# Performance work log

Hardware: AMD Instinct MI355X
Metric: run time of the kernel (lower is better)

Reference implementation:

```python
import jax, jax.numpy as jnp
import numpy as np

N_EMBD = 1024
N_HEAD = 16
HEAD_DIM = N_EMBD // N_HEAD


def setup_inputs() -> dict:
    key = jax.random.key(0)
    ks = jax.random.split(key, 5)
    B, S = 2, 2048
    scale = 0.02
    return {
        "hidden_states": jax.random.normal(ks[0], (B, S, N_EMBD), dtype=jnp.float32),
        "w_attn": jax.random.normal(ks[1], (N_EMBD, 3 * N_EMBD), dtype=jnp.float32) * scale,
        "b_attn": jnp.zeros((3 * N_EMBD,), dtype=jnp.float32),
        "w_proj": jax.random.normal(ks[2], (N_EMBD, N_EMBD), dtype=jnp.float32) * scale,
        "b_proj": jnp.zeros((N_EMBD,), dtype=jnp.float32),
    }


def reference(hidden_states, w_attn, b_attn, w_proj, b_proj):
    B, S, _ = hidden_states.shape
    qkv = hidden_states @ w_attn + b_attn                     # [B,S,3E]
    q, k, v = jnp.split(qkv, 3, axis=-1)                      # each [B,S,E]

    def split_heads(t):  # [B,S,E] -> [B,H,S,D]
        return t.reshape(B, S, N_HEAD, HEAD_DIM).transpose(0, 2, 1, 3)

    q, k, v = split_heads(q), split_heads(k), split_heads(v)

    scores = jnp.einsum("bhqd,bhkd->bhqk", q, k) / np.sqrt(HEAD_DIM).astype(np.float32)
    causal = jnp.tril(jnp.ones((S, S), dtype=bool))
    scores = jnp.where(causal[None, None], scores, jnp.float32(-jnp.inf))
    attn = jax.nn.softmax(scores, axis=-1)                    # [B,H,S,S]
    out = jnp.einsum("bhqk,bhkd->bhqd", attn, v)              # [B,H,S,D]
    out = out.transpose(0, 2, 1, 3).reshape(B, S, N_EMBD)     # merge heads
    out = out @ w_proj + b_proj
    return out
```

## Files before the change

kernel.cpp:

```cpp
#include <hip/hip_runtime.h>
#include <hip/hip_bf16.h>


typedef __attribute__((ext_vector_type(4))) float  float4v;
typedef __attribute__((ext_vector_type(8))) short  short8v;
typedef __attribute__((ext_vector_type(4))) short  short4v;

#define ATT_SCALE 0.18033688011112042f

__device__ __forceinline__ short f2bf(float f) {
  union { float f; unsigned u; } v; v.f = f;
  unsigned r = v.u + 0x7fffu + ((v.u >> 16) & 1u);
  return (short)(r >> 16);
}
__device__ __forceinline__ float bf2f(short s) {
  union { unsigned u; float f; } v; v.u = ((unsigned)(unsigned short)s) << 16;
  return v.f;
}

__device__ __forceinline__ short4v pack_bf16x4(float a, float b, float c, float d) {
  unsigned x0 = __builtin_bit_cast(unsigned, a) + 0x8000u;
  unsigned x1 = __builtin_bit_cast(unsigned, b) + 0x8000u;
  unsigned x2 = __builtin_bit_cast(unsigned, c) + 0x8000u;
  unsigned x3 = __builtin_bit_cast(unsigned, d) + 0x8000u;
  union { unsigned u[2]; short4v s; } r;
  r.u[0] = __builtin_amdgcn_perm(x1, x0, 0x07060302);
  r.u[1] = __builtin_amdgcn_perm(x3, x2, 0x07060302);
  return r.s;
}

__device__ __forceinline__ short4v cvt_pk_bf16x4(float a, float b, float c, float d) {
  union { unsigned u[2]; short4v s; } r;
  asm("v_cvt_pk_bf16_f32 %0, %1, %2" : "=v"(r.u[0]) : "v"(a), "v"(b));
  asm("v_cvt_pk_bf16_f32 %0, %1, %2" : "=v"(r.u[1]) : "v"(c), "v"(d));
  return r.s;
}

__device__ __forceinline__ void gl_lds16(const void* g, void* l) {
  __builtin_amdgcn_global_load_lds(
      (const __attribute__((address_space(1))) unsigned*)g,
      (__attribute__((address_space(3))) unsigned*)l, 16, 0, 0);
}

__global__ __launch_bounds__(256) void prep_kernel(
    const float* __restrict__ hidden, const float* __restrict__ w_attn,
    const float* __restrict__ w_proj, short* __restrict__ hA,
    short* __restrict__ wqkvT, short* __restrict__ wprojT) {
  __shared__ float tile[32][33];
  const int bx = blockIdx.x, t = threadIdx.x;
  if (bx < 4096) {
    const size_t i = ((size_t)bx * 256 + t) * 4;
    float4v v = *(const float4v*)(hidden + i);
    short4v o;
    #pragma unroll
    for (int k = 0; k < 4; k++) o[k] = f2bf(v[k]);
    *(short4v*)(hA + i) = o;
    return;
  }
  const float* in; short* out; int R, C, cx, cy;
  if (bx < 4096 + 3072) {
    in = w_attn; out = wqkvT; R = 1024; C = 3072;
    cx = (bx - 4096) % 96; cy = (bx - 4096) / 96;
  } else {
    in = w_proj; out = wprojT; R = 1024; C = 1024;
    cx = (bx - 7168) % 32; cy = (bx - 7168) / 32;
  }
  const int tx = t & 31, ty = t >> 5;
  const int c0 = cx * 32, r0 = cy * 32;
  #pragma unroll
  for (int i = 0; i < 4; i++)
    tile[ty + i * 8][tx] = in[(size_t)(r0 + ty + i * 8) * C + c0 + tx];
  __syncthreads();
  #pragma unroll
  for (int i = 0; i < 4; i++) {
    const int cc = ty + i * 8;
    out[(size_t)(c0 + cc) * R + r0 + tx] = f2bf(tile[tx][cc]);
  }
}

__global__ __launch_bounds__(512, 2) void gemm_qkv256(
    const short* __restrict__ A, const short* __restrict__ Bt,
    const float* __restrict__ bias, short* __restrict__ qkv,
    short* __restrict__ vA)
{
  __shared__ short As[2][256][64];
  __shared__ short Bs[2][256][64];
  const int K = 1024;
  const int t = threadIdx.x;
  const int lane = t & 63, w = t >> 6;
  const int wm2 = w >> 2, wn4 = w & 3;
  const int l16 = lane & 15, quad = lane >> 4;
  const int e7 = l16 & 7;
  const int row0 = blockIdx.y * 256;
  const int col0 = blockIdx.x * 256;

  float4v acc[8][4] = {};

  const int srow = w * 8 + (lane >> 3);
  const int slog = (lane & 7) ^ (lane >> 3);
  const short* gA = A + (size_t)(row0 + srow) * K + slog * 8;
  const short* gB = Bt + (size_t)(col0 + srow) * K + slog * 8;
  const int sdst = (lane & 7) * 8;

  auto stageA = [&](int b, int qd, int kt) {
    gl_lds16(gA + (size_t)qd * 64 * K + kt * 64,
             &As[b][qd * 64 + w * 8 + (lane >> 3)][sdst]);
  };
  auto stageB = [&](int b, int qd, int kt) {
    gl_lds16(gB + (size_t)qd * 64 * K + kt * 64,
             &Bs[b][qd * 64 + w * 8 + (lane >> 3)][sdst]);
  };

  short8v af[4], bf0[4], bf1[4];
  auto ldA = [&](int b, int mh, int ks) {
    #pragma unroll
    for (int m = 0; m < 4; m++) {
      const int row = wm2 * 128 + mh * 64 + m * 16 + l16;
      af[m] = *(const short8v*)&As[b][row][((ks * 4 + quad) ^ e7) * 8];
    }
  };
  auto ldB = [&](short8v* bf, int b, int ks) {
    #pragma unroll
    for (int n = 0; n < 4; n++) {
      const int row = wn4 * 64 + n * 16 + l16;
      bf[n] = *(const short8v*)&Bs[b][row][((ks * 4 + quad) ^ e7) * 8];
    }
  };
  auto mm = [&](int mb, short8v* bf) {
    __builtin_amdgcn_s_setprio(1);
    #pragma unroll
    for (int m = 0; m < 4; m++)
      #pragma unroll
      for (int n = 0; n < 4; n++)
        acc[mb + m][n] =
            __builtin_amdgcn_mfma_f32_16x16x32_bf16(af[m], bf[n], acc[mb + m][n], 0, 0, 0);
    __builtin_amdgcn_s_setprio(0);
  };
  auto sync_mfma = [&]() {
    __builtin_amdgcn_sched_barrier(0);
    __builtin_amdgcn_s_barrier();
    asm volatile("s_waitcnt lgkmcnt(0)" ::: "memory");
    __builtin_amdgcn_sched_barrier(0);
  };
  auto endp = [&]() {
    __builtin_amdgcn_sched_barrier(0);
    __builtin_amdgcn_s_barrier();
    __builtin_amdgcn_sched_barrier(0);
  };

  #pragma unroll
  for (int qd = 0; qd < 4; qd++) stageA(0, qd, 0);
  #pragma unroll
  for (int qd = 0; qd < 4; qd++) stageB(0, qd, 0);
  #pragma unroll
  for (int qd = 0; qd < 4; qd++) stageB(1, qd, 1);
  asm volatile("s_waitcnt vmcnt(4)" ::: "memory");
  __builtin_amdgcn_s_barrier();
  __builtin_amdgcn_sched_barrier(0);

  const int NIT = K / 128;
  #pragma unroll 1
  for (int it = 0; it < NIT; it++) {
    const bool st = (it < NIT - 1);
    const int t1 = 2 * it + 1, t2 = 2 * it + 2, t3 = 2 * it + 3;

    ldA(0, 0, 0); ldB(bf0, 0, 0);
    stageA(1, 0, t1); stageA(1, 1, t1);
    sync_mfma(); mm(0, bf0); endp();
    ldA(0, 0, 1); ldB(bf1, 0, 1);
    stageA(1, 2, t1); stageA(1, 3, t1);
    sync_mfma(); mm(0, bf1); endp();
    ldA(0, 1, 0);
    if (st) { stageB(0, 0, t2); stageB(0, 1, t2); }
    sync_mfma(); mm(4, bf0); endp();
    ldA(0, 1, 1);
    if (st) { stageB(0, 2, t2); stageB(0, 3, t2); }
    if (st) asm volatile("s_waitcnt vmcnt(4)" ::: "memory");
    else    asm volatile("s_waitcnt vmcnt(0)" ::: "memory");
    sync_mfma(); mm(4, bf1); endp();

    ldA(1, 0, 0); ldB(bf0, 1, 0);
    if (st) { stageA(0, 0, t2); stageA(0, 1, t2); }
    sync_mfma(); mm(0, bf0); endp();
    ldA(1, 0, 1); ldB(bf1, 1, 1);
    if (st) { stageA(0, 2, t2); stageA(0, 3, t2); }
    sync_mfma(); mm(0, bf1); endp();
    ldA(1, 1, 0);
    if (st) { stageB(1, 0, t3); stageB(1, 1, t3); }
    sync_mfma(); mm(4, bf0); endp();
    ldA(1, 1, 1);
    if (st) { stageB(1, 2, t3); stageB(1, 3, t3); }
    if (st) asm volatile("s_waitcnt vmcnt(4)" ::: "memory");
    sync_mfma(); mm(4, bf1); endp();
  }

  if (col0 >= 2048) {
    const int b  = row0 >> 11;
    const int hh = ((col0 - 2048) >> 6) + wn4;
    #pragma unroll
    for (int ktl = 0; ktl < 2; ktl++) {
      const int kt = ((row0 & 2047) >> 6) + wm2 * 2 + ktl;
      short* vbase = vA + ((size_t)((b * 16 + hh) * 32 + kt) * 8) * 512;
      #pragma unroll
      for (int j = 0; j < 4; j++) {
        const float bv = bias[col0 + wn4 * 64 + j * 16 + l16];
        #pragma unroll
        for (int kwp = 0; kwp < 2; kwp++) {
          short8v s8;
          #pragma unroll
          for (int kw = 0; kw < 2; kw++) {
            const int mi = ktl * 4 + kwp * 2 + kw;
            short4v q4 = pack_bf16x4(acc[mi][j][0] + bv, acc[mi][j][1] + bv,
                                     acc[mi][j][2] + bv, acc[mi][j][3] + bv);
            #pragma unroll
            for (int r = 0; r < 4; r++) s8[kw * 4 + r] = q4[r];
          }
          *(short8v*)(vbase + ((size_t)(kwp * 4 + j) * 64 + lane) * 8) = s8;
        }
      }
    }
    return;
  }
  #pragma unroll
  for (int j = 0; j < 4; j++) {
    const int col = col0 + wn4 * 64 + j * 16 + l16;
    const float sc = (col < 1024) ? ATT_SCALE : 1.0f;
    const float bv = bias[col];
    #pragma unroll
    for (int mi = 0; mi < 8; mi++) {
      #pragma unroll
      for (int r = 0; r < 4; r++) {
        const int row = row0 + wm2 * 128 + mi * 16 + quad * 4 + r;
        qkv[(size_t)row * 3072 + col] = f2bf((acc[mi][j][r] + bv) * sc);
      }
    }
  }
}

template<int RB, int MODE>
__global__ __launch_bounds__(256) void gemm_bt(
    const short* __restrict__ A, const short* __restrict__ Bt,
    const float* __restrict__ bias, void* __restrict__ Cout,
    short* __restrict__ vA, int M, int N, int K)
{
  __shared__ short As[3][RB][32];
  __shared__ short Bs[3][128][32];
  const int MI = RB / 32;
  const int t    = threadIdx.x;
  const int lane = t & 63;
  const int wave = t >> 6;
  const int wm   = (wave >> 1) * (RB / 2);
  const int wn   = (wave & 1) * 64;
  const int l16  = lane & 15;
  const int quad = lane >> 4;
  const int row0 = blockIdx.y * RB;
  const int col0 = blockIdx.x * 128;

  float4v acc[MI][4] = {};

  const int srow = lane >> 2;
  const int scol = (lane & 3) * 8;
  const int gcol = ((lane & 3) ^ ((srow >> 1) & 3)) * 8;
  const int rquad = (quad ^ ((l16 >> 1) & 3)) * 8;

  const short* gA0 = A + (size_t)(row0 + wave * ((RB == 128) ? 32 : 16) + srow) * K + gcol;
  const short* gA1 = gA0 + (size_t)16 * K;
  const short* gB0 = Bt + (size_t)(col0 + wave * 32 + srow) * K + gcol;
  const short* gB1 = gB0 + (size_t)16 * K;

  const int NI = K / 32;

  auto stage = [&](int kt, int b) {
    const int k0 = kt * 32;
    if (RB == 128) {
      gl_lds16(gA0 + k0, &As[b][wave * 32 + srow][scol]);
      gl_lds16(gA1 + k0, &As[b][wave * 32 + 16 + srow][scol]);
    } else {
      gl_lds16(gA0 + k0, &As[b][(wave * 16 + srow) & (RB - 1)][scol]);
    }
    gl_lds16(gB0 + k0, &Bs[b][wave * 32 + srow][scol]);
    gl_lds16(gB1 + k0, &Bs[b][wave * 32 + 16 + srow][scol]);
  };

  stage(0, 0);
  stage(1, 1);
  if (RB == 128) asm volatile("s_waitcnt vmcnt(4)" ::: "memory");
  else           asm volatile("s_waitcnt vmcnt(3)" ::: "memory");
  __builtin_amdgcn_s_barrier();
  __builtin_amdgcn_sched_barrier(0);

  int buf = 0;
  for (int i = 0; i < NI; i++) {
    if (i + 2 < NI) stage(i + 2, (buf + 2 >= 3) ? buf - 1 : buf + 2);

    short8v af[MI], bf[4];
    #pragma unroll
    for (int ii = 0; ii < MI; ii++)
      af[ii] = *(const short8v*)&As[buf][wm + ii * 16 + l16][rquad];
    #pragma unroll
    for (int j = 0; j < 4; j++)
      bf[j] = *(const short8v*)&Bs[buf][wn + j * 16 + l16][rquad];
    #pragma unroll
    for (int ii = 0; ii < MI; ii++)
      #pragma unroll
      for (int j = 0; j < 4; j++)
        acc[ii][j] = __builtin_amdgcn_mfma_f32_16x16x32_bf16(af[ii], bf[j], acc[ii][j], 0, 0, 0);

    if (i + 1 < NI) {
      if (i + 2 < NI) {
        if (RB == 128) asm volatile("s_waitcnt vmcnt(4)" ::: "memory");
        else           asm volatile("s_waitcnt vmcnt(3)" ::: "memory");
      } else {
        asm volatile("s_waitcnt vmcnt(0)" ::: "memory");
      }
      __builtin_amdgcn_s_barrier();
      __builtin_amdgcn_sched_barrier(0);
    }
    buf = (buf >= 2) ? 0 : buf + 1;
  }

  #pragma unroll
  for (int j = 0; j < 4; j++) {
    const int col = col0 + wn + j * 16 + l16;
    const float bv = bias[col];
    #pragma unroll
    for (int i = 0; i < MI; i++) {
      #pragma unroll
      for (int r = 0; r < 4; r++) {
        const int row = row0 + wm + i * 16 + quad * 4 + r;
        ((float*)Cout)[(size_t)row * N + col] = acc[i][j][r] + bv;
      }
    }
  }
}

__global__ __launch_bounds__(128, 3) void attn_mfma(
    const short* __restrict__ qkv, const short* __restrict__ vA,
    short* __restrict__ P0, short* __restrict__ P1, float* __restrict__ lp)
{
  __shared__ short KA[2][8 * 512];

  const int bh = blockIdx.x;
  const int b = bh >> 4, h = bh & 15;
  const int s = 79 - blockIdx.y;
  int qt = 0, sbase = 0;
  for (;;) { const int nc = (qt >> 3) + 1; if (s < sbase + nc) break; sbase += nc; qt++; }
  const int c = s - sbase;
  const int kt0  = c * 8;
  const int kend = min(qt + 1, kt0 + 8);

  const int t = threadIdx.x;
  const int lane = t & 63, w = t >> 6;
  const int l16 = lane & 15, quad = lane >> 4;

  const size_t base = (size_t)b * 2048 * 3072;
  const int qoff = h * 64, koff = 1024 + h * 64;

  int qg[2];
  short8v qf[2][2];
  #pragma unroll
  for (int hh = 0; hh < 2; hh++) {
    qg[hh] = qt * 64 + w * 32 + hh * 16 + l16;
    #pragma unroll
    for (int ks = 0; ks < 2; ks++)
      qf[hh][ks] = *(const short8v*)(qkv + base + (size_t)qg[hh] * 3072
                                     + qoff + ks * 32 + quad * 8);
  }

  float4v O[2][4] = {};
  float l[2] = {0.0f, 0.0f};

  const short* kgw = qkv + base + (size_t)l16 * 3072 + koff + w * 32 + quad * 8;
  const short* vg  = vA + (size_t)(bh * 32) * 4096 + lane * 8;

  auto stageK = [&](int kt, int buf) {
    #pragma unroll
    for (int j = 0; j < 4; j++)
      gl_lds16(kgw + ((size_t)kt * 64 + j * 16) * 3072,
               &KA[buf][(w * 4 + j) * 512 + lane * 8]);
  };

  stageK(kt0, 0);

  for (int kt = kt0; kt < kend; kt++) {
    const int buf = (kt - kt0) & 1;
    __syncthreads();

    short8v vv[8];
    #pragma unroll
    for (int id = 0; id < 8; id++)
      vv[id] = *(const short8v*)(vg + (size_t)kt * 4096 + id * 512);

    if (kt + 1 < kend) stageK(kt + 1, buf ^ 1);

    float4v sv[2][4] = {};
    __builtin_amdgcn_s_setprio(1);
    #pragma unroll
    for (int ks = 0; ks < 2; ks++)
      #pragma unroll
      for (int jm = 0; jm < 4; jm++) {
        const short8v kf = *(const short8v*)&KA[buf][(ks * 4 + jm) * 512 + lane * 8];
        #pragma unroll
        for (int hh = 0; hh < 2; hh++)
          sv[hh][jm] = __builtin_amdgcn_mfma_f32_16x16x32_bf16(kf, qf[hh][ks],
                                                               sv[hh][jm], 0, 0, 0);
      }
    __builtin_amdgcn_s_setprio(0);

    if (kt == qt) {
      #pragma unroll
      for (int hh = 0; hh < 2; hh++)
        #pragma unroll
        for (int jm = 0; jm < 4; jm++) {
          const int kv = kt * 64 + jm * 16 + quad * 4;
          #pragma unroll
          for (int r = 0; r < 4; r++)
            if (kv + r > qg[hh]) sv[hh][jm][r] = -INFINITY;
        }
    }

    short4v pk[2][4];
    #pragma unroll
    for (int hh = 0; hh < 2; hh++)
      #pragma unroll
      for (int jm = 0; jm < 4; jm++) {
        float p0 = __builtin_amdgcn_exp2f(sv[hh][jm][0]);
        float p1 = __builtin_amdgcn_exp2f(sv[hh][jm][1]);
        float p2 = __builtin_amdgcn_exp2f(sv[hh][jm][2]);
        float p3 = __builtin_amdgcn_exp2f(sv[hh][jm][3]);
        l[hh] += (p0 + p1) + (p2 + p3);
        pk[hh][jm] = cvt_pk_bf16x4(p0, p1, p2, p3);
      }

    __builtin_amdgcn_s_setprio(1);
    #pragma unroll
    for (int id = 0; id < 8; id++) {
      const int kwp = id >> 2, dm = id & 3;
      const short8v v8 = vv[id];
      const short4v v0 = {v8[0], v8[1], v8[2], v8[3]};
      const short4v v1 = {v8[4], v8[5], v8[6], v8[7]};
      #pragma unroll
      for (int hh = 0; hh < 2; hh++) {
        O[hh][dm] = __builtin_amdgcn_mfma_f32_16x16x16bf16_1k(v0, pk[hh][kwp * 2],
                                                              O[hh][dm], 0, 0, 0);
        O[hh][dm] = __builtin_amdgcn_mfma_f32_16x16x16bf16_1k(v1, pk[hh][kwp * 2 + 1],
                                                              O[hh][dm], 0, 0, 0);
      }
    }
    __builtin_amdgcn_s_setprio(0);
  }

  #pragma unroll
  for (int hh = 0; hh < 2; hh++) {
    l[hh] += __shfl_xor(l[hh], 16);
    l[hh] += __shfl_xor(l[hh], 32);
  }
  const int i = bh * 80 + s;
  short* pp = (i < 2048) ? (P0 + (size_t)i * 4096) : (P1 + (size_t)(i - 2048) * 4096);
  #pragma unroll
  for (int hh = 0; hh < 2; hh++) {
    const int row = w * 32 + hh * 16 + l16;
    if (quad == 0) lp[(size_t)i * 64 + row] = l[hh];
    short* pr = pp + row * 64;
    #pragma unroll
    for (int dm = 0; dm < 4; dm++)
      *(short4v*)(pr + dm * 16 + quad * 4) =
          pack_bf16x4(O[hh][dm][0], O[hh][dm][1], O[hh][dm][2], O[hh][dm][3]);
  }
}

__global__ __launch_bounds__(256) void merge_attn(
    const short* __restrict__ P0, const short* __restrict__ P1,
    const float* __restrict__ lp, short* __restrict__ aout)
{
  const int idx = blockIdx.x * 256 + threadIdx.x;
  const int q = idx >> 7;
  const int rest = idx & 127;
  const int h  = rest >> 3;
  const int dg = (rest & 7) * 8;
  const int b  = q >> 11;
  const int qr = q & 2047;
  const int qt = qr >> 6;
  const int row = qr & 63;
  const int a = qt >> 3, bq = qt & 7;
  const int off = qt + 4 * a * (a - 1) + a * bq;
  const int nc  = a + 1;
  const int bh  = b * 16 + h;

  float acc[8] = {};
  float suml = 0.0f;
  for (int c = 0; c < nc; c++) {
    const int i = bh * 80 + off + c;
    const short* pp = (i < 2048) ? (P0 + (size_t)i * 4096) : (P1 + (size_t)(i - 2048) * 4096);
    const short8v o = *(const short8v*)(pp + row * 64 + dg);
    #pragma unroll
    for (int k = 0; k < 8; k++) acc[k] += bf2f(o[k]);
    suml += lp[(size_t)i * 64 + row];
  }
  const float inv = 1.0f / suml;
  short8v ov;
  #pragma unroll
  for (int k = 0; k < 8; k++) ov[k] = f2bf(acc[k] * inv);
  *(short8v*)(aout + (size_t)q * 1024 + h * 64 + dg) = ov;
}

extern "C" void kernel_launch(void* const* d_in, const int* in_sizes, int n_in,
                              void* d_out, int out_size, void* d_ws, size_t ws_size,
                              hipStream_t stream) {
  const float* hidden = (const float*)d_in[0];
  const float* w_attn = (const float*)d_in[1];
  const float* b_attn = (const float*)d_in[2];
  const float* w_proj = (const float*)d_in[3];
  const float* b_proj = (const float*)d_in[4];
  float* outp = (float*)d_out;

  char* ws = (char*)d_ws;
  short* hA     = (short*)(ws);
  float* lp     = (float*)(ws + 8ull  * 1024 * 1024);
  short* wqkvT  = (short*)(ws + 8ull  * 1024 * 1024);
  short* wprojT = (short*)(ws + 14ull * 1024 * 1024);
  short* qkvb   = (short*)(ws + 16ull * 1024 * 1024);
  short* vAbuf  = (short*)(ws + 40ull * 1024 * 1024);
  short* aout   = (short*)(ws + 40ull * 1024 * 1024);
  short* P0     = (short*)d_out;

  prep_kernel<<<8192, 256, 0, stream>>>(hidden, w_attn, w_proj, hA, wqkvT, wprojT);
  gemm_qkv256<<<dim3(12, 16), 512, 0, stream>>>(hA, wqkvT, b_attn, qkvb, vAbuf);
  attn_mfma<<<dim3(32, 80), 128, 0, stream>>>(qkvb, vAbuf, P0, hA, lp);
  merge_attn<<<2048, 256, 0, stream>>>(P0, hA, lp, aout);
  gemm_bt<64, 0><<<dim3(8, 64), 256, 0, stream>>>(aout, wprojT, b_proj, outp, nullptr, 4096, 1024, 1024);
}
```

Baseline: 184.3 us.

## Replace projection GEMM with 128x128 tile, K=64 double-buffered pipelined kernel

Swaps the generic 64-row projection GEMM for a dedicated 128x128-tile kernel with 64-wide K slices, double-buffered LDS, an XOR swizzle, and staged global-to-LDS loads interleaved with MFMA phases under setprio. The aim is more reuse per loaded tile and better overlap of loads with matrix math in the output projection. In exchange the grid shrinks to 256 blocks, which may underfill the GPU's compute units, and the hand-tuned waitcnt schedule adds complexity.

```diff
diff --git a/kernel.cpp b/kernel.cpp
--- a/kernel.cpp
+++ b/kernel.cpp
@@ -237,98 +237,131 @@
   }
 }
 
-template<int RB, int MODE>
-__global__ __launch_bounds__(256) void gemm_bt(
+__global__ __launch_bounds__(256, 2) void gemm_proj128(
     const short* __restrict__ A, const short* __restrict__ Bt,
-    const float* __restrict__ bias, void* __restrict__ Cout,
-    short* __restrict__ vA, int M, int N, int K)
+    const float* __restrict__ bias, float* __restrict__ Cout)
 {
-  __shared__ short As[3][RB][32];
-  __shared__ short Bs[3][128][32];
-  const int MI = RB / 32;
-  const int t    = threadIdx.x;
-  const int lane = t & 63;
-  const int wave = t >> 6;
-  const int wm   = (wave >> 1) * (RB / 2);
-  const int wn   = (wave & 1) * 64;
-  const int l16  = lane & 15;
-  const int quad = lane >> 4;
-  const int row0 = blockIdx.y * RB;
+  __shared__ short As[2][128][64];
+  __shared__ short Bs[2][128][64];
+  const int K = 1024;
+  const int t = threadIdx.x;
+  const int lane = t & 63, w = t >> 6;
+  const int wm2 = w >> 1, wn2 = w & 1;
+  const int l16 = lane & 15, quad = lane >> 4;
+  const int e7 = l16 & 7;
+  const int row0 = blockIdx.y * 128;
   const int col0 = blockIdx.x * 128;
 
-  float4v acc[MI][4] = {};
-
-  const int srow = lane >> 2;
-  const int scol = (lane & 3) * 8;
-  const int gcol = ((lane & 3) ^ ((srow >> 1) & 3)) * 8;
-  const int rquad = (quad ^ ((l16 >> 1) & 3)) * 8;
-
-  const short* gA0 = A + (size_t)(row0 + wave * ((RB == 128) ? 32 : 16) + srow) * K + gcol;
-  const short* gA1 = gA0 + (size_t)16 * K;
-  const short* gB0 = Bt + (size_t)(col0 + wave * 32 + srow) * K + gcol;
-  const short* gB1 = gB0 + (size_t)16 * K;
-
-  const int NI = K / 32;
-
-  auto stage = [&](int kt, int b) {
-    const int k0 = kt * 32;
-    if (RB == 128) {
-      gl_lds16(gA0 + k0, &As[b][wave * 32 + srow][scol]);
-      gl_lds16(gA1 + k0, &As[b][wave * 32 + 16 + srow][scol]);
-    } else {
-      gl_lds16(gA0 + k0, &As[b][(wave * 16 + srow) & (RB - 1)][scol]);
-    }
-    gl_lds16(gB0 + k0, &Bs[b][wave * 32 + srow][scol]);
-    gl_lds16(gB1 + k0, &Bs[b][wave * 32 + 16 + srow][scol]);
-  };
-
-  stage(0, 0);
-  stage(1, 1);
-  if (RB == 128) asm volatile("s_waitcnt vmcnt(4)" ::: "memory");
-  else           asm volatile("s_waitcnt vmcnt(3)" ::: "memory");
+  float4v acc[4][4] = {};
+
+  const int srow = w * 8 + (lane >> 3);
+  const int slog = (lane & 7) ^ (lane >> 3);
+  const short* gA = A + (size_t)(row0 + srow) * K + slog * 8;
+  const short* gB = Bt + (size_t)(col0 + srow) * K + slog * 8;
+  const int sdst = (lane & 7) * 8;
+
+  auto stageA = [&](int b, int qd, int kt) {
+    gl_lds16(gA + (size_t)qd * 32 * K + kt * 64,
+             &As[b][qd * 32 + w * 8 + (lane >> 3)][sdst]);
+  };
+  auto stageB = [&](int b, int qd, int kt) {
+    gl_lds16(gB + (size_t)qd * 32 * K + kt * 64,
+             &Bs[b][qd * 32 + w * 8 + (lane >> 3)][sdst]);
+  };
+
+  short8v af[2], bf0[4], bf1[4];
+  auto ldA = [&](int b, int mh, int ks) {
+    #pragma unroll
+    for (int m = 0; m < 2; m++) {
+      const int row = wm2 * 64 + mh * 32 + m * 16 + l16;
+      af[m] = *(const short8v*)&As[b][row][((ks * 4 + quad) ^ e7) * 8];
+    }
+  };
+  auto ldB = [&](short8v* bf, int b, int ks) {
+    #pragma unroll
+    for (int n = 0; n < 4; n++) {
+      const int row = wn2 * 64 + n * 16 + l16;
+      bf[n] = *(const short8v*)&Bs[b][row][((ks * 4 + quad) ^ e7) * 8];
+    }
+  };
+  auto mm = [&](int mb, short8v* bf) {
+    __builtin_amdgcn_s_setprio(1);
+    #pragma unroll
+    for (int m = 0; m < 2; m++)
+      #pragma unroll
+      for (int n = 0; n < 4; n++)
+        acc[mb + m][n] =
+            __builtin_amdgcn_mfma_f32_16x16x32_bf16(af[m], bf[n], acc[mb + m][n], 0, 0, 0);
+    __builtin_amdgcn_s_setprio(0);
+  };
+  auto sync_mfma = [&]() {
+    __builtin_amdgcn_sched_barrier(0);
+    __builtin_amdgcn_s_barrier();
+    asm volatile("s_waitcnt lgkmcnt(0)" ::: "memory");
+    __builtin_amdgcn_sched_barrier(0);
+  };
+  auto endp = [&]() {
+    __builtin_amdgcn_sched_barrier(0);
+    __builtin_amdgcn_s_barrier();
+    __builtin_amdgcn_sched_barrier(0);
+  };
+
+  #pragma unroll
+  for (int qd = 0; qd < 4; qd++) stageA(0, qd, 0);
+  #pragma unroll
+  for (int qd = 0; qd < 4; qd++) stageB(0, qd, 0);
+  #pragma unroll
+  for (int qd = 0; qd < 4; qd++) stageB(1, qd, 1);
+  asm volatile("s_waitcnt vmcnt(4)" ::: "memory");
   __builtin_amdgcn_s_barrier();
   __builtin_amdgcn_sched_barrier(0);
 
-  int buf = 0;
-  for (int i = 0; i < NI; i++) {
-    if (i + 2 < NI) stage(i + 2, (buf + 2 >= 3) ? buf - 1 : buf + 2);
-
-    short8v af[MI], bf[4];
-    #pragma unroll
-    for (int ii = 0; ii < MI; ii++)
-      af[ii] = *(const short8v*)&As[buf][wm + ii * 16 + l16][rquad];
-    #pragma unroll
-    for (int j = 0; j < 4; j++)
-      bf[j] = *(const short8v*)&Bs[buf][wn + j * 16 + l16][rquad];
-    #pragma unroll
-    for (int ii = 0; ii < MI; ii++)
-      #pragma unroll
-      for (int j = 0; j < 4; j++)
-        acc[ii][j] = __builtin_amdgcn_mfma_f32_16x16x32_bf16(af[ii], bf[j], acc[ii][j], 0, 0, 0);
-
-    if (i + 1 < NI) {
-      if (i + 2 < NI) {
-        if (RB == 128) asm volatile("s_waitcnt vmcnt(4)" ::: "memory");
-        else           asm volatile("s_waitcnt vmcnt(3)" ::: "memory");
-      } else {
-        asm volatile("s_waitcnt vmcnt(0)" ::: "memory");
-      }
-      __builtin_amdgcn_s_barrier();
-      __builtin_amdgcn_sched_barrier(0);
-    }
-    buf = (buf >= 2) ? 0 : buf + 1;
+  const int NIT = K / 128;
+  #pragma unroll 1
+  for (int it = 0; it < NIT; it++) {
+    const bool st = (it < NIT - 1);
+    const int t1 = 2 * it + 1, t2 = 2 * it + 2, t3 = 2 * it + 3;
+
+    ldA(0, 0, 0); ldB(bf0, 0, 0);
+    stageA(1, 0, t1); stageA(1, 1, t1);
+    sync_mfma(); mm(0, bf0); endp();
+    ldA(0, 0, 1); ldB(bf1, 0, 1);
+    stageA(1, 2, t1); stageA(1, 3, t1);
+    sync_mfma(); mm(0, bf1); endp();
+    ldA(0, 1, 0);
+    if (st) { stageB(0, 0, t2); stageB(0, 1, t2); }
+    sync_mfma(); mm(2, bf0); endp();
+    ldA(0, 1, 1);
+    if (st) { stageB(0, 2, t2); stageB(0, 3, t2); }
+    if (st) asm volatile("s_waitcnt vmcnt(4)" ::: "memory");
+    else    asm volatile("s_waitcnt vmcnt(0)" ::: "memory");
+    sync_mfma(); mm(2, bf1); endp();
+
+    ldA(1, 0, 0); ldB(bf0, 1, 0);
+    if (st) { stageA(0, 0, t2); stageA(0, 1, t2); }
+    sync_mfma(); mm(0, bf0); endp();
+    ldA(1, 0, 1); ldB(bf1, 1, 1);
+    if (st) { stageA(0, 2, t2); stageA(0, 3, t2); }
+    sync_mfma(); mm(0, bf1); endp();
+    ldA(1, 1, 0);
+    if (st) { stageB(1, 0, t3); stageB(1, 1, t3); }
+    sync_mfma(); mm(2, bf0); endp();
+    ldA(1, 1, 1);
+    if (st) { stageB(1, 2, t3); stageB(1, 3, t3); }
+    if (st) asm volatile("s_waitcnt vmcnt(4)" ::: "memory");
+    sync_mfma(); mm(2, bf1); endp();
   }
 
   #pragma unroll
   for (int j = 0; j < 4; j++) {
-    const int col = col0 + wn + j * 16 + l16;
+    const int col = col0 + wn2 * 64 + j * 16 + l16;
     const float bv = bias[col];
     #pragma unroll
-    for (int i = 0; i < MI; i++) {
+    for (int mi = 0; mi < 4; mi++) {
       #pragma unroll
       for (int r = 0; r < 4; r++) {
-        const int row = row0 + wm + i * 16 + quad * 4 + r;
-        ((float*)Cout)[(size_t)row * N + col] = acc[i][j][r] + bv;
+        const int row = row0 + wm2 * 64 + mi * 16 + quad * 4 + r;
+        Cout[(size_t)row * 1024 + col] = acc[mi][j][r] + bv;
       }
     }
   }
@@ -528,5 +561,5 @@
   gemm_qkv256<<<dim3(12, 16), 512, 0, stream>>>(hA, wqkvT, b_attn, qkvb, vAbuf);
   attn_mfma<<<dim3(32, 80), 128, 0, stream>>>(qkvb, vAbuf, P0, hA, lp);
   merge_attn<<<2048, 256, 0, stream>>>(P0, hA, lp, aout);
-  gemm_bt<64, 0><<<dim3(8, 64), 256, 0, stream>>>(aout, wprojT, b_proj, outp, nullptr, 4096, 1024, 1024);
-}
+  gemm_proj128<<<dim3(8, 32), 256, 0, stream>>>(aout, wprojT, b_proj, outp);
+}
```

New measurement: 186.6 us. Within noise of the previous version (+1.3%).
